# Optimization experiments

Hardware: AMD Instinct MI355X
Metric: run time of the kernel (lower is better)

Reference implementation:

```python
import jax, jax.numpy as jnp
import numpy as np

B, L, D = 256, 64, 1024


def setup_inputs() -> dict:
    key = jax.random.key(0)
    k0, k1, k2, k3, k4, k5, k6 = jax.random.split(key, 7)
    left = jax.random.normal(k0, (B, L, D), jnp.float32)
    right = jax.random.normal(k1, (B, L, D), jnp.float32)
    s = 1.0 / np.sqrt(L)  # torch Linear default init bound
    Wl = jax.random.uniform(k2, (L, L), jnp.float32, -s, s)
    bl = jax.random.uniform(k3, (L,), jnp.float32, -s, s)
    Wr = jax.random.uniform(k4, (L, L), jnp.float32, -s, s)
    br = jax.random.uniform(k5, (L,), jnp.float32, -s, s)
    sc = 1.0 / np.sqrt(2 * L * 3)  # Conv1d(2L->L, k=3) default init bound
    Wconv = jax.random.uniform(k6, (L, 2 * L, 3), jnp.float32, -sc, sc)
    return {"left": left, "right": right, "Wl": Wl, "bl": bl,
            "Wr": Wr, "br": br, "Wconv": Wconv}


def reference(left, right, Wl, bl, Wr, br, Wconv):
    Bd, Ld, Dd = left.shape
    # nn.Linear(L,L) over the length axis: y[b,k,d] = sum_l x[b,l,d] * W[k,l] + b[k]
    left = jnp.einsum('bld,kl->bkd', left, Wl) + bl[None, :, None]
    right = jnp.einsum('bld,kl->bkd', right, Wr) + br[None, :, None]
    # The 2L-step python loop computes, for i in [0, 2L):
    #   out[:, i, :] = sum_j left[:, j, :] * right[:, j + (L-1) - i, :]  (in-range j)
    # i.e. a full cross-correlation along the length axis (last row all zeros).
    # lax conv IS cross-correlation, so run one grouped conv over B*D channels.
    lhs = left.transpose(0, 2, 1).reshape(1, Bd * Dd, Ld)    # [1, B*D, L]  (NCW)
    rhs = right.transpose(0, 2, 1).reshape(Bd * Dd, 1, Ld)   # [B*D, 1, L]  (OIW)
    corr = jax.lax.conv_general_dilated(
        lhs, rhs, window_strides=(1,), padding=[(Ld - 1, Ld - 1)],
        dimension_numbers=('NCW', 'OIW', 'NCW'),
        feature_group_count=Bd * Dd)                          # [1, B*D, 2L-1]
    corr = jnp.pad(corr, ((0, 0), (0, 0), (0, 1)))            # last shift is all-zero
    out = corr.reshape(Bd, Dd, 2 * Ld).transpose(0, 2, 1)     # [B, 2L, D]
    # nn.Conv1d(2L -> L, kernel_size=3, padding=1, bias=False), width = D
    y = jax.lax.conv_general_dilated(
        out, Wconv, window_strides=(1,), padding=[(1, 1)],
        dimension_numbers=('NCW', 'OIW', 'NCW'))              # [B, L, D]
    return y
```

## Files before the change

kernel.cpp:

```cpp
#include <hip/hip_runtime.h>

#define DD 1024
#define TD 62
#define NTILE 17
#define BB 256

typedef __attribute__((ext_vector_type(8))) short short8;
typedef __attribute__((ext_vector_type(4))) float float4_;

__device__ __forceinline__ unsigned short f2bf(float f) {
    union { float f; unsigned u; } v; v.f = f;
    unsigned u = v.u;
    return (unsigned short)((u + 0x7fffu + ((u >> 16) & 1u)) >> 16);
}
__device__ __forceinline__ unsigned pack2(float a, float b) {
    return (unsigned)f2bf(a) | ((unsigned)f2bf(b) << 16);
}
__device__ __forceinline__ unsigned packh2(float a, float b) {
    union { _Float16 h[2]; unsigned u; } v;
    v.h[0] = (_Float16)a; v.h[1] = (_Float16)b;
    return v.u;
}
__device__ __forceinline__ float h2f_lo(unsigned u) {
    union { unsigned u; _Float16 h[2]; } v; v.u = u; return (float)v.h[0];
}
__device__ __forceinline__ float h2f_hi(unsigned u) {
    union { unsigned u; _Float16 h[2]; } v; v.u = u; return (float)v.h[1];
}

__global__ void prep_w(const float* __restrict__ Wconv,
                       const float* __restrict__ Wl,
                       const float* __restrict__ Wr,
                       unsigned short* __restrict__ W2) {
    int o = blockIdx.x * 256 + threadIdx.x;
    if (o < 24576) {
        int j = o & 7, lane = (o >> 3) & 63, w = (o >> 9) & 3, q = (o >> 11) & 3, t = o >> 13;
        int m = lane & 15, quad = lane >> 4;
        int k = 16 * w + m, c = 32 * q + 8 * quad + j;
        W2[o] = f2bf(Wconv[(k * 128 + c) * 3 + t]);
    } else {
        int o2 = o - 24576;
        int j = o2 & 7, lane = (o2 >> 3) & 63, mt = (o2 >> 9) & 3,
            l0s = (o2 >> 11) & 1, mat = (o2 >> 12) & 1;
        int m = lane & 15, quad = lane >> 4;
        int k = 16 * mt + m, l = 32 * l0s + quad * 8 + j;
        const float* src = mat ? Wr : Wl;
        W2[o] = f2bf(src[k * 64 + l]);
    }
}

template<int W>
__device__ __forceinline__ void corrAB(const unsigned* __restrict__ Lh, const float (&Rr)[64],
                                       float (&accA)[16], float (&accB)[16], int lane) {
#pragma unroll
    for (int ii = 0; ii < 16; ++ii) { accA[ii] = 0.0f; accB[ii] = 0.0f; }
#pragma unroll
    for (int j2 = 0; j2 < 32; ++j2) {
        unsigned u = Lh[j2 * 64 + (lane ^ (((j2 >> 1) & 1) << 4))];
        float Lj0 = h2f_lo(u), Lj1 = h2f_hi(u);
#pragma unroll
        for (int jj = 0; jj < 2; ++jj) {
            const int j = 2 * j2 + jj;
            const float Lj = jj ? Lj1 : Lj0;
#pragma unroll
            for (int ii = 0; ii < 16; ++ii) {
                const int i = 16 * W + ii;
                if (j <= i) accA[ii] += Lj * Rr[j + 63 - i];
                else        accB[ii] += Lj * Rr[j - 1 - i];
            }
        }
    }
}

template<bool PRE>
__global__ __launch_bounds__(256, 3)
void fused_cc_kernel(const float* __restrict__ left,
                     const float* __restrict__ right,
                     const float* __restrict__ Wl,
                     const float* __restrict__ bl,
                     const float* __restrict__ Wr,
                     const float* __restrict__ br,
                     const float* __restrict__ Wconv,
                     const unsigned short* __restrict__ W2,
                     float* __restrict__ out) {
    __shared__ unsigned shm[8192];
    unsigned* xL = shm;
    unsigned* xR = shm + 2048;
    unsigned* Lh = shm + 4096;
    unsigned* Rh = shm + 6144;
    unsigned short* corrT = (unsigned short*)shm;

    const int tid  = threadIdx.x;
    const int lane = tid & 63;
    const int w    = __builtin_amdgcn_readfirstlane(tid >> 6);
    const int kw   = 16 * w;
    const int m16  = lane & 15;
    const int quad = lane >> 4;

    const int b       = blockIdx.y;
    const int d_start = blockIdx.x * TD;
    const int ncols   = min(TD, DD - d_start);

    const int  g        = d_start - 1 + lane;
    const bool colvalid = (g >= 0) && (g < DD);

    const float* lb = left  + (size_t)b * 64 * DD;
    const float* rb = right + (size_t)b * 64 * DD;

    short8 afL[2], afR[2];
    if (PRE) {
        const short8* Wf = (const short8*)(W2 + 24576);
        afL[0] = Wf[(0 * 4 + w) * 64 + lane];
        afL[1] = Wf[(1 * 4 + w) * 64 + lane];
        afR[0] = Wf[(2 * 4 + w) * 64 + lane];
        afR[1] = Wf[(3 * 4 + w) * 64 + lane];
    } else {
#pragma unroll
        for (int l0s = 0; l0s < 2; ++l0s) {
            const float* pL = Wl + (kw + m16) * 64 + 32 * l0s + quad * 8;
            const float* pR = Wr + (kw + m16) * 64 + 32 * l0s + quad * 8;
#pragma unroll
            for (int j = 0; j < 8; ++j) {
                afL[l0s][j] = (short)f2bf(pL[j]);
                afR[l0s][j] = (short)f2bf(pR[j]);
            }
        }
    }
    float blv[4], brv[4];
#pragma unroll
    for (int r = 0; r < 4; ++r) {
        int krow = kw + quad * 4 + r;
        blv[r] = bl[krow]; brv[r] = br[krow];
    }

#pragma unroll
    for (int i = 0; i < 8; ++i) {
        int p = 8 * w + i, l = 2 * p;
        float a0 = colvalid ? lb[l * DD + g] : 0.0f;
        float a1 = colvalid ? lb[(l + 1) * DD + g] : 0.0f;
        float c0 = colvalid ? rb[l * DD + g] : 0.0f;
        float c1 = colvalid ? rb[(l + 1) * DD + g] : 0.0f;
        int pc = lane ^ (((p >> 2) & 1) << 4);
        xL[p * 64 + pc] = pack2(a0, a1);
        xR[p * 64 + pc] = pack2(c0, c1);
    }
    __syncthreads();

    float4_ accL[4], accR[4];
#pragma unroll
    for (int nt = 0; nt < 4; ++nt) { accL[nt] = (float4_){0,0,0,0}; accR[nt] = (float4_){0,0,0,0}; }
#pragma unroll
    for (int l0s = 0; l0s < 2; ++l0s)
#pragma unroll
        for (int nt = 0; nt < 4; ++nt) {
            union { unsigned u[4]; short8 s; } tL, tR;
#pragma unroll
            for (int jj = 0; jj < 4; ++jj) {
                int row = l0s * 16 + quad * 4 + jj;
                int col = (nt * 16 + m16) ^ (((row >> 2) & 1) << 4);
                int a = row * 64 + col;
                tL.u[jj] = xL[a];
                tR.u[jj] = xR[a];
            }
            accL[nt] = __builtin_amdgcn_mfma_f32_16x16x32_bf16(afL[l0s], tL.s, accL[nt], 0, 0, 0);
            accR[nt] = __builtin_amdgcn_mfma_f32_16x16x32_bf16(afR[l0s], tR.s, accR[nt], 0, 0, 0);
        }

#pragma unroll
    for (int nt = 0; nt < 4; ++nt) {
        int col = nt * 16 + m16;
        int k2  = 8 * w + 2 * quad;
        int c0 = col ^ ((quad & 1) << 4);
        Lh[k2 * 64 + c0]       = packh2(accL[nt][0] + blv[0], accL[nt][1] + blv[1]);
        Lh[(k2 + 1) * 64 + c0] = packh2(accL[nt][2] + blv[2], accL[nt][3] + blv[3]);
        Rh[k2 * 64 + c0]       = packh2(accR[nt][0] + brv[0], accR[nt][1] + brv[1]);
        Rh[(k2 + 1) * 64 + c0] = packh2(accR[nt][2] + brv[2], accR[nt][3] + brv[3]);
    }
    __syncthreads();

    float Rr[64];
#pragma unroll
    for (int k2 = 0; k2 < 32; ++k2) {
        unsigned u = Rh[k2 * 64 + (lane ^ (((k2 >> 1) & 1) << 4))];
        Rr[2 * k2]     = h2f_lo(u);
        Rr[2 * k2 + 1] = h2f_hi(u);
    }

    float accA[16], accB[16];
    switch (w) {
        case 0: corrAB<0>(Lh, Rr, accA, accB, lane); break;
        case 1: corrAB<1>(Lh, Rr, accA, accB, lane); break;
        case 2: corrAB<2>(Lh, Rr, accA, accB, lane); break;
        default: corrAB<3>(Lh, Rr, accA, accB, lane); break;
    }

    short8 af[12];
#pragma unroll
    for (int t = 0; t < 3; ++t)
#pragma unroll
        for (int qi = 0; qi < 4; ++qi) {
            if (PRE) {
                af[t * 4 + qi] = ((const short8*)W2)[((t * 4 + qi) * 4 + w) * 64 + lane];
            } else {
                const float* p = Wconv + ((kw + m16) * 128 + 32 * qi + 8 * quad) * 3 + t;
#pragma unroll
                for (int j = 0; j < 8; ++j) af[t * 4 + qi][j] = (short)f2bf(p[3 * j]);
            }
        }

    {
        const float* srcs[4] = { accA, accA + 8, accB, accB + 8 };
        const int grps[4] = { 2 * w, 2 * w + 1, 8 + 2 * w, 8 + 2 * w + 1 };
#pragma unroll
        for (int s = 0; s < 4; ++s) {
            short8 v;
#pragma unroll
            for (int j = 0; j < 8; ++j) v[j] = colvalid ? (short)f2bf(srcs[s][j]) : (short)0;
            int phys = grps[s] ^ (lane & 7);
            *(short8*)&corrT[lane * 128 + phys * 8] = v;
        }
    }
    __syncthreads();

    float4_ yacc[4];
#pragma unroll
    for (int nt = 0; nt < 4; ++nt) yacc[nt] = (float4_){0,0,0,0};
#pragma unroll
    for (int t = 0; t < 3; ++t)
#pragma unroll
        for (int qi = 0; qi < 4; ++qi)
#pragma unroll
            for (int nt = 0; nt < 4; ++nt) {
                int row  = nt * 16 + m16 + t;
                int phys = (4 * qi + quad) ^ (row & 7);
                short8 bf = *(const short8*)&corrT[row * 128 + phys * 8];
                yacc[nt] = __builtin_amdgcn_mfma_f32_16x16x32_bf16(af[t * 4 + qi], bf,
                                                                   yacc[nt], 0, 0, 0);
            }

#pragma unroll
    for (int nt = 0; nt < 4; ++nt) {
        const int dd = nt * 16 + m16;
        if (dd < ncols) {
#pragma unroll
            for (int r = 0; r < 4; ++r) {
                int k = kw + 4 * quad + r;
                out[((size_t)b * 64 + k) * DD + d_start + dd] = yacc[nt][r];
            }
        }
    }
}

extern "C" void kernel_launch(void* const* d_in, const int* in_sizes, int n_in,
                              void* d_out, int out_size, void* d_ws, size_t ws_size,
                              hipStream_t stream) {
    const float* left  = (const float*)d_in[0];
    const float* right = (const float*)d_in[1];
    const float* Wl    = (const float*)d_in[2];
    const float* bl    = (const float*)d_in[3];
    const float* Wr    = (const float*)d_in[4];
    const float* br    = (const float*)d_in[5];
    const float* Wconv = (const float*)d_in[6];
    float* out = (float*)d_out;

    dim3 grid(NTILE, BB);
    if (ws_size >= 32768 * sizeof(unsigned short)) {
        unsigned short* W2 = (unsigned short*)d_ws;
        prep_w<<<128, 256, 0, stream>>>(Wconv, Wl, Wr, W2);
        fused_cc_kernel<true><<<grid, dim3(256), 0, stream>>>(left, right, Wl, bl, Wr, br,
                                                              Wconv, W2, out);
    } else {
        fused_cc_kernel<false><<<grid, dim3(256), 0, stream>>>(left, right, Wl, bl, Wr, br,
                                                               Wconv, nullptr, out);
    }
}
```

Before: 256.1 us.

## Compute length-axis correlation with packed fp16 dot2 and triangular-balanced passes

```diff
diff --git a/kernel.cpp b/kernel.cpp
--- a/kernel.cpp
+++ b/kernel.cpp
@@ -7,6 +7,7 @@
 
 typedef __attribute__((ext_vector_type(8))) short short8;
 typedef __attribute__((ext_vector_type(4))) float float4_;
+typedef _Float16 half2_ __attribute__((ext_vector_type(2)));
 
 __device__ __forceinline__ unsigned short f2bf(float f) {
     union { float f; unsigned u; } v; v.f = f;
@@ -21,11 +22,14 @@
     v.h[0] = (_Float16)a; v.h[1] = (_Float16)b;
     return v.u;
 }
-__device__ __forceinline__ float h2f_lo(unsigned u) {
-    union { unsigned u; _Float16 h[2]; } v; v.u = u; return (float)v.h[0];
-}
-__device__ __forceinline__ float h2f_hi(unsigned u) {
-    union { unsigned u; _Float16 h[2]; } v; v.u = u; return (float)v.h[1];
+__device__ __forceinline__ float fdot2f(unsigned a, unsigned b, float c) {
+#if __has_builtin(__builtin_amdgcn_fdot2)
+    union { unsigned u; half2_ h; } ua, ub; ua.u = a; ub.u = b;
+    return __builtin_amdgcn_fdot2(ua.h, ub.h, c, false);
+#else
+    union { unsigned u; _Float16 h[2]; } ua, ub; ua.u = a; ub.u = b;
+    return c + (float)ua.h[0] * (float)ub.h[0] + (float)ua.h[1] * (float)ub.h[1];
+#endif
 }
 
 __global__ void prep_w(const float* __restrict__ Wconv,
@@ -49,27 +53,62 @@
     }
 }
 
-template<int W>
-__device__ __forceinline__ void corrAB(const unsigned* __restrict__ Lh, const float (&Rr)[64],
-                                       float (&accA)[16], float (&accB)[16], int lane) {
-#pragma unroll
-    for (int ii = 0; ii < 16; ++ii) { accA[ii] = 0.0f; accB[ii] = 0.0f; }
-#pragma unroll
-    for (int j2 = 0; j2 < 32; ++j2) {
-        unsigned u = Lh[j2 * 64 + (lane ^ (((j2 >> 1) & 1) << 4))];
-        float Lj0 = h2f_lo(u), Lj1 = h2f_hi(u);
-#pragma unroll
-        for (int jj = 0; jj < 2; ++jj) {
-            const int j = 2 * j2 + jj;
-            const float Lj = jj ? Lj1 : Lj0;
-#pragma unroll
-            for (int ii = 0; ii < 16; ++ii) {
-                const int i = 16 * W + ii;
-                if (j <= i) accA[ii] += Lj * Rr[j + 63 - i];
-                else        accB[ii] += Lj * Rr[j - 1 - i];
-            }
-        }
-    }
+template<int NJ2, bool ODD, bool REV>
+__device__ __forceinline__ void corr_pass(const unsigned* __restrict__ X,
+                                          const unsigned* __restrict__ Y,
+                                          int q, int climit, int G,
+                                          int lane, bool colvalid,
+                                          unsigned short* __restrict__ corrT) {
+    constexpr int SAFE = (NJ2 == 32) ? 20 : 4;
+    unsigned P[NJ2 + 1];
+    const unsigned* Yq = Y + q * 64;
+#pragma unroll
+    for (int t2 = 0; t2 <= NJ2; ++t2) {
+        unsigned v = Yq[t2 * 64 + (lane ^ ((((t2 >> 1) & 1)) << 4))];
+        if (t2 >= SAFE) { if (t2 + q >= 32) v = 0u; }
+        P[t2] = v;
+    }
+    unsigned AL[NJ2];
+#pragma unroll
+    for (int t2 = 0; t2 < NJ2; ++t2)
+        AL[t2] = (P[t2] >> 16) | (P[t2 + 1] << 16);
+
+    float acc[8];
+#pragma unroll
+    for (int u = 0; u < 8; ++u) acc[u] = 0.0f;
+
+#pragma unroll
+    for (int c = 0; c < NJ2 / 4; ++c) {
+        if (c < climit) {
+            unsigned xp[4];
+#pragma unroll
+            for (int jj = 0; jj < 4; ++jj) {
+                int j2 = 4 * c + jj;
+                xp[jj] = X[j2 * 64 + (lane ^ ((((j2 >> 1) & 1)) << 4))];
+            }
+#pragma unroll
+            for (int jj = 0; jj < 4; ++jj) {
+                int j2 = 4 * c + jj;
+#pragma unroll
+                for (int u = 0; u < 8; ++u) {
+                    if (j2 < NJ2 - (u >> 1)) {
+                        unsigned yv;
+                        if (!ODD) yv = (u & 1) ? AL[j2 + (u >> 1)] : P[j2 + (u >> 1)];
+                        else      yv = (u & 1) ? P[j2 + (u >> 1) + 1] : AL[j2 + (u >> 1)];
+                        acc[u] = fdot2f(xp[jj], yv, acc[u]);
+                    }
+                }
+            }
+        }
+    }
+    short8 v;
+#pragma unroll
+    for (int u = 0; u < 8; ++u) {
+        int jg = REV ? (7 - u) : u;
+        v[jg] = colvalid ? (short)f2bf(acc[u]) : (short)0;
+    }
+    int phys = G ^ (lane & 7);
+    *(short8*)&corrT[lane * 128 + phys * 8] = v;
 }
 
 template<bool PRE>
@@ -83,7 +122,7 @@
                      const float* __restrict__ Wconv,
                      const unsigned short* __restrict__ W2,
                      float* __restrict__ out) {
-    __shared__ unsigned shm[8192];
+    __shared__ unsigned shm[9088];
     unsigned* xL = shm;
     unsigned* xR = shm + 2048;
     unsigned* Lh = shm + 4096;
@@ -178,21 +217,10 @@
     }
     __syncthreads();
 
-    float Rr[64];
-#pragma unroll
-    for (int k2 = 0; k2 < 32; ++k2) {
-        unsigned u = Rh[k2 * 64 + (lane ^ (((k2 >> 1) & 1) << 4))];
-        Rr[2 * k2]     = h2f_lo(u);
-        Rr[2 * k2 + 1] = h2f_hi(u);
-    }
-
-    float accA[16], accB[16];
-    switch (w) {
-        case 0: corrAB<0>(Lh, Rr, accA, accB, lane); break;
-        case 1: corrAB<1>(Lh, Rr, accA, accB, lane); break;
-        case 2: corrAB<2>(Lh, Rr, accA, accB, lane); break;
-        default: corrAB<3>(Lh, Rr, accA, accB, lane); break;
-    }
+    corr_pass<32, false, true >(Lh, Rh, 4 * w,      8 - w, 7 - w,  lane, colvalid, corrT);
+    corr_pass<16, false, true >(Lh, Rh, 28 - 4 * w, w + 1, w,      lane, colvalid, corrT);
+    corr_pass<32, true,  false>(Rh, Lh, 4 * w,      8 - w, 8 + w,  lane, colvalid, corrT);
+    corr_pass<16, true,  false>(Rh, Lh, 28 - 4 * w, w + 1, 15 - w, lane, colvalid, corrT);
 
     short8 af[12];
 #pragma unroll
@@ -207,19 +235,6 @@
                 for (int j = 0; j < 8; ++j) af[t * 4 + qi][j] = (short)f2bf(p[3 * j]);
             }
         }
-
-    {
-        const float* srcs[4] = { accA, accA + 8, accB, accB + 8 };
-        const int grps[4] = { 2 * w, 2 * w + 1, 8 + 2 * w, 8 + 2 * w + 1 };
-#pragma unroll
-        for (int s = 0; s < 4; ++s) {
-            short8 v;
-#pragma unroll
-            for (int j = 0; j < 8; ++j) v[j] = colvalid ? (short)f2bf(srcs[s][j]) : (short)0;
-            int phys = grps[s] ^ (lane & 7);
-            *(short8*)&corrT[lane * 128 + phys * 8] = v;
-        }
-    }
     __syncthreads();
 
     float4_ yacc[4];
```

New measurement: 226.5 us. -11.5%, faster.
